# Kernel tuning notes

Measured on AMD Instinct MI355X. Metric: run time of the kernel, lower is better.

Reference implementation:

```python
import jax, jax.numpy as jnp
import numpy as np

C = 64
CQ = C // 4
G = 8  # group norm groups
EPS_GN = 1e-5
POS_COEF = 0.1


def setup_inputs() -> dict:
    key = jax.random.key(0)
    ks = jax.random.split(key, 12)
    B, N = 2, 4096
    return {
        "context_features": jax.random.normal(ks[0], (B, C, N), jnp.float32),
        "motion_features": jax.random.normal(ks[1], (B, C, N), jnp.float32),
        "xyz1": jax.random.uniform(ks[2], (B, N, 3), jnp.float32),
        # tied q/k conv weight (Conv1d k=1, no bias): (C//4, C)
        "Wqk": jax.random.normal(ks[3], (CQ, C), jnp.float32) * 0.1,
        # v_conv: Conv1d(C, C, 1) with bias
        "Wv": jax.random.normal(ks[4], (C, C), jnp.float32) * 0.1,
        "bv": jax.random.normal(ks[5], (C,), jnp.float32) * 0.1,
        # trans_conv: Conv1d(C, C, 1) with bias
        "Wt": jax.random.normal(ks[6], (C, C), jnp.float32) * 0.1,
        "bt": jax.random.normal(ks[7], (C,), jnp.float32) * 0.1,
        # GroupNorm(8, C) affine params
        "gn_w": jax.random.normal(ks[8], (C,), jnp.float32) * 0.1 + 1.0,
        "gn_b": jax.random.normal(ks[9], (C,), jnp.float32) * 0.1,
        # PReLU single slope, alpha_gma scalar (init 0 in torch; random here for testing)
        "prelu_a": jnp.float32(0.25) + jax.random.normal(ks[10], (), jnp.float32) * 0.01,
        "alpha": jax.random.normal(ks[11], (), jnp.float32) * 0.1,
    }


def _group_norm(x, w, b):
    # x: (B, C, N)
    B, Cc, N = x.shape
    xg = x.reshape(B, G, Cc // G, N)
    mu = xg.mean(axis=(2, 3), keepdims=True)
    var = xg.var(axis=(2, 3), keepdims=True)
    xn = ((xg - mu) * jax.lax.rsqrt(var + EPS_GN)).reshape(B, Cc, N)
    return xn * w[None, :, None] + b[None, :, None]


def reference(context_features, motion_features, xyz1, Wqk, Wv, bv, Wt, bt, gn_w, gn_b, prelu_a, alpha):
    # --- self attention (tied q/k) ---
    q = jnp.einsum("oc,bcn->bon", Wqk, context_features)  # (B, C/4, N)
    corr = jnp.einsum("bom,bon->bmn", q, q)               # (B, N, N)
    attn = jax.nn.softmax(corr, axis=-1)
    attn = attn / (1e-9 + attn.sum(axis=1, keepdims=True))

    # --- position mask via Gram-trick squared distances ---
    sq = jnp.sum(xyz1 * xyz1, axis=-1)                    # (B, N)
    d = sq[:, :, None] + sq[:, None, :] - 2.0 * jnp.einsum("bid,bjd->bij", xyz1, xyz1)
    d = jnp.maximum(d, 0.0)
    pos_am = d / (1e-9 + d.sum(axis=1, keepdims=True))
    mask = pos_am <= POS_COEF

    local = attn * mask
    local = jax.nn.softmax(local, axis=-1)
    local = local / (1e-9 + local.sum(axis=1, keepdims=True))
    attn = attn + local

    # --- GMA fusion ---
    xv = jnp.einsum("oc,bcn->bon", Wv, motion_features) + bv[None, :, None]
    gma = jnp.einsum("bcm,bmn->bcn", xv, attn)
    res = jnp.einsum("oc,bcn->bon", Wt, motion_features - gma) + bt[None, :, None]
    gr = _group_norm(res, gn_w, gn_b)
    gr = jnp.where(gr >= 0, gr, prelu_a * gr)  # PReLU
    return alpha * gr + motion_features
```

## Files before the change

### kernel.cpp

```cpp
#include <hip/hip_runtime.h>
#include <hip/hip_bf16.h>
#include <cstdio>

#define NB 2
#define NN 4096
#define NC 64
#define NQ 16
#define POS_COEF 0.1f

#define OFF_QT   0u
#define OFF_QK   131072u
#define OFF_XYZ4 262144u
#define OFF_XYZK 294912u
#define OFF_IRS1 327680u
#define OFF_IRS2 335872u
#define OFF_THR  344064u
#define OFF_ICS1 352256u
#define OFF_FLAG 360448u
#define OFF_XVB  360464u
#define OFF_SUMS 622608u
#define OFF_GN   622616u
#define OFF_CS2  622648u
#define OFF_GMA  630840u
#define OFF_G2   1155128u
#define WS_TOTAL 1679416u
#define ZERO_F   (WS_TOTAL - OFF_SUMS)
#define OFF_A0   1679424u
#define OFF_AE   18456640u
#define FULL_F   35233856u

using bf16x8 = __attribute__((ext_vector_type(8))) short;
using f32x4v = __attribute__((ext_vector_type(4))) float;

__device__ __forceinline__ float rcpf_(float x) { return __builtin_amdgcn_rcpf(x); }
__device__ __forceinline__ unsigned short f2bf(float x) {
  __hip_bfloat16 h = __float2bfloat16(x);
  return *(unsigned short*)&h;
}
__device__ __forceinline__ float bf2f(unsigned short u) {
  unsigned v = ((unsigned)u) << 16;
  return __builtin_bit_cast(float, v);
}

__device__ __forceinline__ float ldin(const void* p, size_t i, bool f32) {
  return f32 ? ((const float*)p)[i]
             : __bfloat162float(((const __hip_bfloat16*)p)[i]);
}

#define DOT16M(A0,A1,A2,A3,B0,B1,B2,B3) \
  fmaf((A0).x,(B0).x, fmaf((A0).y,(B0).y, fmaf((A0).z,(B0).z, fmaf((A0).w,(B0).w, \
  fmaf((A1).x,(B1).x, fmaf((A1).y,(B1).y, fmaf((A1).z,(B1).z, fmaf((A1).w,(B1).w, \
  fmaf((A2).x,(B2).x, fmaf((A2).y,(B2).y, fmaf((A2).z,(B2).z, fmaf((A2).w,(B2).w, \
  fmaf((A3).x,(B3).x, fmaf((A3).y,(B3).y, fmaf((A3).z,(B3).z, (A3).w*(B3).w)))))))))))))))

#define DOTC(M0,M1,M2,M3,C) \
  fmaf((M0).x,k0.C, fmaf((M0).y,k1.C, fmaf((M0).z,k2.C, fmaf((M0).w,k3.C, \
  fmaf((M1).x,k4.C, fmaf((M1).y,k5.C, fmaf((M1).z,k6.C, fmaf((M1).w,k7.C, \
  fmaf((M2).x,k8.C, fmaf((M2).y,k9.C, fmaf((M2).z,k10.C, fmaf((M2).w,k11.C, \
  fmaf((M3).x,k12.C, fmaf((M3).y,k13.C, fmaf((M3).z,k14.C, (M3).w*k15.C)))))))))))))))

#define LKPL(base, n0) \
  const float4 k0  = *(const float4*)((base) + 0*NN  + (n0)); \
  const float4 k1  = *(const float4*)((base) + 1*NN  + (n0)); \
  const float4 k2  = *(const float4*)((base) + 2*NN  + (n0)); \
  const float4 k3  = *(const float4*)((base) + 3*NN  + (n0)); \
  const float4 k4  = *(const float4*)((base) + 4*NN  + (n0)); \
  const float4 k5  = *(const float4*)((base) + 5*NN  + (n0)); \
  const float4 k6  = *(const float4*)((base) + 6*NN  + (n0)); \
  const float4 k7  = *(const float4*)((base) + 7*NN  + (n0)); \
  const float4 k8  = *(const float4*)((base) + 8*NN  + (n0)); \
  const float4 k9  = *(const float4*)((base) + 9*NN  + (n0)); \
  const float4 k10 = *(const float4*)((base) + 10*NN + (n0)); \
  const float4 k11 = *(const float4*)((base) + 11*NN + (n0)); \
  const float4 k12 = *(const float4*)((base) + 12*NN + (n0)); \
  const float4 k13 = *(const float4*)((base) + 13*NN + (n0)); \
  const float4 k14 = *(const float4*)((base) + 14*NN + (n0)); \
  const float4 k15 = *(const float4*)((base) + 15*NN + (n0));

#define WRED(s) { s += __shfl_xor(s, 32); s += __shfl_xor(s, 16); \
  s += __shfl_xor(s, 8); s += __shfl_xor(s, 4); s += __shfl_xor(s, 2); s += __shfl_xor(s, 1); }

#define LQROW(v, base) \
  const float4 v##0 = *(const float4*)((base)); \
  const float4 v##1 = *(const float4*)((base) + 4); \
  const float4 v##2 = *(const float4*)((base) + 8); \
  const float4 v##3 = *(const float4*)((base) + 12);

__global__ __launch_bounds__(256) void k0_detect(
    const unsigned short* __restrict__ ctx_u16, float* __restrict__ flag) {
  const int tid = threadIdx.x;
  int bad = 0;
  for (int i = tid; i < 8192; i += 256) {
    const unsigned short u = ctx_u16[i];
    const int e = (u >> 7) & 0xFF;
    if (e >= 134 || (e >= 1 && e <= 100)) bad++;
  }
  __shared__ int cnt;
  if (tid == 0) cnt = 0;
  __syncthreads();
  atomicAdd(&cnt, bad);
  __syncthreads();
  if (tid == 0) flag[0] = (cnt > 256) ? 1.0f : 0.0f;
}

__global__ __launch_bounds__(256) void k1_q_xyz(
    const void* __restrict__ ctx, const void* __restrict__ xyz,
    const void* __restrict__ wqk, const float* __restrict__ flag,
    float* __restrict__ qt, float* __restrict__ qk,
    float* __restrict__ xyz4, float* __restrict__ xyzk,
    float* __restrict__ sums) {
  const bool f32 = flag[0] > 0.5f;
  const int tid = threadIdx.x;
// ... 65 lines not shown
  float4 a1 = *(const float4*)(bvs + og * 16 + 4);
  float4 a2 = *(const float4*)(bvs + og * 16 + 8);
  float4 a3 = *(const float4*)(bvs + og * 16 + 12);
  const size_t mbase = (size_t)b * 64 * NN + n;
#pragma unroll 4
  for (int c = 0; c < 64; ++c) {
    float x = ldin(mot, mbase + (size_t)c * NN, f32);
    const float4 w0 = *(const float4*)(wvT + c * 64 + og * 16 + 0);
    const float4 w1 = *(const float4*)(wvT + c * 64 + og * 16 + 4);
    const float4 w2 = *(const float4*)(wvT + c * 64 + og * 16 + 8);
    const float4 w3 = *(const float4*)(wvT + c * 64 + og * 16 + 12);
    a0.x = fmaf(w0.x, x, a0.x); a0.y = fmaf(w0.y, x, a0.y); a0.z = fmaf(w0.z, x, a0.z); a0.w = fmaf(w0.w, x, a0.w);
    a1.x = fmaf(w1.x, x, a1.x); a1.y = fmaf(w1.y, x, a1.y); a1.z = fmaf(w1.z, x, a1.z); a1.w = fmaf(w1.w, x, a1.w);
    a2.x = fmaf(w2.x, x, a2.x); a2.y = fmaf(w2.y, x, a2.y); a2.z = fmaf(w2.z, x, a2.z); a2.w = fmaf(w2.w, x, a2.w);
    a3.x = fmaf(w3.x, x, a3.x); a3.y = fmaf(w3.y, x, a3.y); a3.z = fmaf(w3.z, x, a3.z); a3.w = fmaf(w3.w, x, a3.w);
  }
  unsigned short* xb = xvb + (size_t)b * 64 * NN + n;
  const int o0 = og * 16;
  xb[(size_t)(o0 + 0) * NN] = f2bf(a0.x);  xb[(size_t)(o0 + 1) * NN] = f2bf(a0.y);
  xb[(size_t)(o0 + 2) * NN] = f2bf(a0.z);  xb[(size_t)(o0 + 3) * NN] = f2bf(a0.w);
  xb[(size_t)(o0 + 4) * NN] = f2bf(a1.x);  xb[(size_t)(o0 + 5) * NN] = f2bf(a1.y);
  xb[(size_t)(o0 + 6) * NN] = f2bf(a1.z);  xb[(size_t)(o0 + 7) * NN] = f2bf(a1.w);
  xb[(size_t)(o0 + 8) * NN] = f2bf(a2.x);  xb[(size_t)(o0 + 9) * NN] = f2bf(a2.y);
  xb[(size_t)(o0 +10) * NN] = f2bf(a2.z);  xb[(size_t)(o0 +11) * NN] = f2bf(a2.w);
  xb[(size_t)(o0 +12) * NN] = f2bf(a3.x);  xb[(size_t)(o0 +13) * NN] = f2bf(a3.y);
  xb[(size_t)(o0 +14) * NN] = f2bf(a3.z);  xb[(size_t)(o0 +15) * NN] = f2bf(a3.w);
}

__global__ __launch_bounds__(256) void k2b_thr(
    const float* __restrict__ xyz4, const float* __restrict__ sums,
    float* __restrict__ thr) {
  const int idx = blockIdx.x * 256 + threadIdx.x;
  const int b = idx >> 12;
  const float4 pn = *(const float4*)(xyz4 + (size_t)idx * 4);
  const float Px = sums[b * 4 + 0], Py = sums[b * 4 + 1];
  const float Pz = sums[b * 4 + 2], S1 = sums[b * 4 + 3];
  float csd = fmaf((float)NN, pn.w, S1)
            - 2.f * (pn.x * Px + pn.y * Py + pn.z * Pz);
  thr[idx] = POS_COEF * (1e-9f + csd);
}


__global__ __launch_bounds__(256) void p1_rs1(
    const float* __restrict__ qt, const float* __restrict__ qk,
    float* __restrict__ irs1) {
  const int tid = threadIdx.x;
  const int b = blockIdx.x >> 8;
  const int m0 = (blockIdx.x & 255) << 4;
  const int w = tid >> 6, lane = tid & 63;
  const float* qb = qt + (size_t)b * NN * 16;
  const float* kb = qk + (size_t)b * 16 * NN;
  const int mA = m0 + w, mB = m0 + w + 4, mC = m0 + w + 8, mD = m0 + w + 12;
  LQROW(ma, qb + (size_t)mA * 16)
  LQROW(mb, qb + (size_t)mB * 16)
  LQROW(mc, qb + (size_t)mC * 16)
  LQROW(md, qb + (size_t)mD * 16)
  float sA = 0.f, sB = 0.f, sC = 0.f, sD = 0.f;
  for (int it = 0; it < 16; ++it) {
    const int n0 = (it << 8) + (lane << 2);
    LKPL(kb, n0)
    sA += __expf(fminf(DOTC(ma0,ma1,ma2,ma3,x), 80.f));
    sA += __expf(fminf(DOTC(ma0,ma1,ma2,ma3,y), 80.f));
    sA += __expf(fminf(DOTC(ma0,ma1,ma2,ma3,z), 80.f));
    sA += __expf(fminf(DOTC(ma0,ma1,ma2,ma3,w), 80.f));
    sB += __expf(fminf(DOTC(mb0,mb1,mb2,mb3,x), 80.f));
    sB += __expf(fminf(DOTC(mb0,mb1,mb2,mb3,y), 80.f));
    sB += __expf(fminf(DOTC(mb0,mb1,mb2,mb3,z), 80.f));
    sB += __expf(fminf(DOTC(mb0,mb1,mb2,mb3,w), 80.f));
    sC += __expf(fminf(DOTC(mc0,mc1,mc2,mc3,x), 80.f));
    sC += __expf(fminf(DOTC(mc0,mc1,mc2,mc3,y), 80.f));
    sC += __expf(fminf(DOTC(mc0,mc1,mc2,mc3,z), 80.f));
    sC += __expf(fminf(DOTC(mc0,mc1,mc2,mc3,w), 80.f));
    sD += __expf(fminf(DOTC(md0,md1,md2,md3,x), 80.f));
    sD += __expf(fminf(DOTC(md0,md1,md2,md3,y), 80.f));
    sD += __expf(fminf(DOTC(md0,md1,md2,md3,z), 80.f));
    sD += __expf(fminf(DOTC(md0,md1,md2,md3,w), 80.f));
  }
  WRED(sA) WRED(sB) WRED(sC) WRED(sD)
  if (lane == 0) {
    irs1[b * NN + mA] = rcpf_(sA);
    irs1[b * NN + mB] = rcpf_(sB);
    irs1[b * NN + mC] = rcpf_(sC);
    irs1[b * NN + mD] = rcpf_(sD);
  }
}

__global__ __launch_bounds__(256) void p3_rs2(
    const float* __restrict__ qt, const float* __restrict__ qk,
    const float* __restrict__ xyz4, const float* __restrict__ xyzk,
    const float* __restrict__ irs1, const float* __restrict__ ics1,
    const float* __restrict__ thr, float* __restrict__ irs2) {
  const int tid = threadIdx.x;
  const int b = blockIdx.x >> 8;
  const int m0 = (blockIdx.x & 255) << 4;
  const int w = tid >> 6, lane = tid & 63;
  const float* qb = qt + (size_t)b * NN * 16;
  const float* kb = qk + (size_t)b * 16 * NN;
  const float* xk = xyzk + (size_t)b * 4 * NN;
  const int mA = m0 + w, mB = m0 + w + 4, mC = m0 + w + 8, mD = m0 + w + 12;
  LQROW(ma, qb + (size_t)mA * 16)
  LQROW(mb, qb + (size_t)mB * 16)
  LQROW(mc, qb + (size_t)mC * 16)
  LQROW(md, qb + (size_t)mD * 16)
  const float4 pmA = *(const float4*)(xyz4 + ((size_t)b * NN + mA) * 4);
  const float4 pmB = *(const float4*)(xyz4 + ((size_t)b * NN + mB) * 4);
  const float4 pmC = *(const float4*)(xyz4 + ((size_t)b * NN + mC) * 4);
  const float4 pmD = *(const float4*)(xyz4 + ((size_t)b * NN + mD) * 4);
  const float rA = irs1[b * NN + mA];
  const float rB = irs1[b * NN + mB];
  const float rC = irs1[b * NN + mC];
  const float rD = irs1[b * NN + mD];
  float sA = 0.f, sB = 0.f, sC = 0.f, sD = 0.f;
#define P3C(S, M0,M1,M2,M3, PM, R, C) { \
    float corr_ = DOTC(M0,M1,M2,M3,C); \
    float a1v_ = __expf(fminf(corr_, 80.f)) * (R) * ic.C; \
    float dd_ = (PM).w + pw.C - 2.f * ((PM).x * px.C + (PM).y * py.C + (PM).z * pz.C); \
    dd_ = fmaxf(dd_, 0.f); \
    float l0_ = (dd_ <= th.C) ? a1v_ : 0.f; \
    S += __expf(l0_); }
  for (int it = 0; it < 16; ++it) {
    const int n0 = (it << 8) + (lane << 2);
    LKPL(kb, n0)
    const float4 px = *(const float4*)(xk + 0*NN + n0);
    const float4 py = *(const float4*)(xk + 1*NN + n0);
    const float4 pz = *(const float4*)(xk + 2*NN + n0);
    const float4 pw = *(const float4*)(xk + 3*NN + n0);
    const float4 ic = *(const float4*)(ics1 + b * NN + n0);
    const float4 th = *(const float4*)(thr + b * NN + n0);
    P3C(sA, ma0,ma1,ma2,ma3, pmA, rA, x)
    P3C(sA, ma0,ma1,ma2,ma3, pmA, rA, y)
    P3C(sA, ma0,ma1,ma2,ma3, pmA, rA, z)
    P3C(sA, ma0,ma1,ma2,ma3, pmA, rA, w)
    P3C(sB, mb0,mb1,mb2,mb3, pmB, rB, x)
    P3C(sB, mb0,mb1,mb2,mb3, pmB, rB, y)
    P3C(sB, mb0,mb1,mb2,mb3, pmB, rB, z)
    P3C(sB, mb0,mb1,mb2,mb3, pmB, rB, w)
    P3C(sC, mc0,mc1,mc2,mc3, pmC, rC, x)
    P3C(sC, mc0,mc1,mc2,mc3, pmC, rC, y)
    P3C(sC, mc0,mc1,mc2,mc3, pmC, rC, z)
    P3C(sC, mc0,mc1,mc2,mc3, pmC, rC, w)
    P3C(sD, md0,md1,md2,md3, pmD, rD, x)
    P3C(sD, md0,md1,md2,md3, pmD, rD, y)
    P3C(sD, md0,md1,md2,md3, pmD, rD, z)
    P3C(sD, md0,md1,md2,md3, pmD, rD, w)
  }
#undef P3C
  WRED(sA) WRED(sB) WRED(sC) WRED(sD)
  if (lane == 0) {
    irs2[b * NN + mA] = rcpf_(sA);
    irs2[b * NN + mB] = rcpf_(sB);
    irs2[b * NN + mC] = rcpf_(sC);
    irs2[b * NN + mD] = rcpf_(sD);
  }
}

__global__ __launch_bounds__(256) void k7_gma(
    const float* __restrict__ qt, const float* __restrict__ xyz4,
    const unsigned short* __restrict__ xvb,
    const float* __restrict__ irs1, const float* __restrict__ irs2,
    const float* __restrict__ ics1, const float* __restrict__ thr,
    float* __restrict__ g1, float* __restrict__ g2, float* __restrict__ cs2) {
  const int tid = threadIdx.x;
  const int bid = blockIdx.x;
  const int msl = bid & 7;
  const int nb = (bid >> 3) & 63;
  const int b = bid >> 9;
// ... 49 lines not shown
      COMPA(g * 4 + 3, u1.w, u2.w)
      *(ushort4*)(attns1 + ni * 72 + (aw << 4) + (g << 2)) = u1;
      *(ushort4*)(attns2 + ni * 72 + (aw << 4) + (g << 2)) = u2;
    }
    __syncthreads();
#pragma unroll
    for (int h = 0; h < 2; ++h) {
      const bf16x8 a1 = *(const bf16x8*)(attns1 + (nw + lr) * 72 + h * 32 + quad * 8);
      const bf16x8 a2 = *(const bf16x8*)(attns2 + (nw + lr) * 72 + h * 32 + quad * 8);
      const bf16x8 b0 = *(const bf16x8*)(xvs + (lr) * 72 + h * 32 + quad * 8);
      const bf16x8 b1 = *(const bf16x8*)(xvs + (16 + lr) * 72 + h * 32 + quad * 8);
      const bf16x8 b2 = *(const bf16x8*)(xvs + (32 + lr) * 72 + h * 32 + quad * 8);
      const bf16x8 b3 = *(const bf16x8*)(xvs + (48 + lr) * 72 + h * 32 + quad * 8);
      acc0 = __builtin_amdgcn_mfma_f32_16x16x32_bf16(a1, b0, acc0, 0, 0, 0);
      acc1 = __builtin_amdgcn_mfma_f32_16x16x32_bf16(a1, b1, acc1, 0, 0, 0);
      acc2 = __builtin_amdgcn_mfma_f32_16x16x32_bf16(a1, b2, acc2, 0, 0, 0);
      acc3 = __builtin_amdgcn_mfma_f32_16x16x32_bf16(a1, b3, acc3, 0, 0, 0);
      d0 = __builtin_amdgcn_mfma_f32_16x16x32_bf16(a2, b0, d0, 0, 0, 0);
      d1 = __builtin_amdgcn_mfma_f32_16x16x32_bf16(a2, b1, d1, 0, 0, 0);
      d2 = __builtin_amdgcn_mfma_f32_16x16x32_bf16(a2, b2, d2, 0, 0, 0);
      d3 = __builtin_amdgcn_mfma_f32_16x16x32_bf16(a2, b3, d3, 0, 0, 0);
    }
  }
#undef COMPA
  atomicAdd(&cs2[b * NN + na], csacc);
#define EPI(ACC, DST, CT) { \
    float* g_ = (DST) + ((size_t)b * NN + n0 + nw + (quad << 2)) * 64 + (CT) * 16 + lr; \
    atomicAdd(g_ + 0,   ACC[0]); \
    atomicAdd(g_ + 64,  ACC[1]); \
    atomicAdd(g_ + 128, ACC[2]); \
    atomicAdd(g_ + 192, ACC[3]); }
  EPI(acc0, g1, 0) EPI(acc1, g1, 1) EPI(acc2, g1, 2) EPI(acc3, g1, 3)
  EPI(d0, g2, 0) EPI(d1, g2, 1) EPI(d2, g2, 2) EPI(d3, g2, 3)
#undef EPI
}


__global__ __launch_bounds__(256) void p1w_rs1(
    const float* __restrict__ qt, const float* __restrict__ qk,
    float* __restrict__ irs1, unsigned short* __restrict__ a0g) {
  const int tid = threadIdx.x;
  const int b = blockIdx.x >> 8;
  const int m0 = (blockIdx.x & 255) << 4;
  const int w = tid >> 6, lane = tid & 63;
  const float* qb = qt + (size_t)b * NN * 16;
  const float* kb = qk + (size_t)b * 16 * NN;
  unsigned short* ab = a0g + (size_t)b * NN * NN;
  const int mA = m0 + w, mB = m0 + w + 4, mC = m0 + w + 8, mD = m0 + w + 12;
  LQROW(ma, qb + (size_t)mA * 16)
  LQROW(mb, qb + (size_t)mB * 16)
  LQROW(mc, qb + (size_t)mC * 16)
  LQROW(md, qb + (size_t)mD * 16)
  float sA = 0.f, sB = 0.f, sC = 0.f, sD = 0.f;
#define P1E(S, U, UC, M0,M1,M2,M3, C) { \
    float e_ = __expf(fminf(DOTC(M0,M1,M2,M3,C), 80.f)); \
    unsigned short us_ = f2bf(e_); U.UC = us_; S += bf2f(us_); }
  for (int it = 0; it < 16; ++it) {
    const int n0 = (it << 8) + (lane << 2);
    LKPL(kb, n0)
    ushort4 uA, uB, uC, uD;
    P1E(sA, uA, x, ma0,ma1,ma2,ma3, x) P1E(sA, uA, y, ma0,ma1,ma2,ma3, y)
    P1E(sA, uA, z, ma0,ma1,ma2,ma3, z) P1E(sA, uA, w, ma0,ma1,ma2,ma3, w)
    P1E(sB, uB, x, mb0,mb1,mb2,mb3, x) P1E(sB, uB, y, mb0,mb1,mb2,mb3, y)
    P1E(sB, uB, z, mb0,mb1,mb2,mb3, z) P1E(sB, uB, w, mb0,mb1,mb2,mb3, w)
    P1E(sC, uC, x, mc0,mc1,mc2,mc3, x) P1E(sC, uC, y, mc0,mc1,mc2,mc3, y)
    P1E(sC, uC, z, mc0,mc1,mc2,mc3, z) P1E(sC, uC, w, mc0,mc1,mc2,mc3, w)
    P1E(sD, uD, x, md0,md1,md2,md3, x) P1E(sD, uD, y, md0,md1,md2,md3, y)
    P1E(sD, uD, z, md0,md1,md2,md3, z) P1E(sD, uD, w, md0,md1,md2,md3, w)
    *(ushort4*)(ab + (size_t)mA * NN + n0) = uA;
    *(ushort4*)(ab + (size_t)mB * NN + n0) = uB;
    *(ushort4*)(ab + (size_t)mC * NN + n0) = uC;
    *(ushort4*)(ab + (size_t)mD * NN + n0) = uD;
  }
#undef P1E
  WRED(sA) WRED(sB) WRED(sC) WRED(sD)
  if (lane == 0) {
    irs1[b * NN + mA] = rcpf_(sA);
    irs1[b * NN + mB] = rcpf_(sB);
    irs1[b * NN + mC] = rcpf_(sC);
    irs1[b * NN + mD] = rcpf_(sD);
  }
}

__global__ __launch_bounds__(256) void p3w_rs2(
    const float* __restrict__ xyz4, const float* __restrict__ xyzk,
    const float* __restrict__ irs1, const float* __restrict__ ics1,
    const float* __restrict__ thr, float* __restrict__ irs2,
    const unsigned short* __restrict__ a0g, unsigned short* __restrict__ aeg) {
  const int tid = threadIdx.x;
  const int b = blockIdx.x >> 8;
  const int m0 = (blockIdx.x & 255) << 4;
  const int w = tid >> 6, lane = tid & 63;
  const float* xk = xyzk + (size_t)b * 4 * NN;
  const unsigned short* ab = a0g + (size_t)b * NN * NN;
  unsigned short* eb = aeg + (size_t)b * NN * NN;
  const int mA = m0 + w, mB = m0 + w + 4, mC = m0 + w + 8, mD = m0 + w + 12;
  const float4 pmA = *(const float4*)(xyz4 + ((size_t)b * NN + mA) * 4);
  const float4 pmB = *(const float4*)(xyz4 + ((size_t)b * NN + mB) * 4);
  const float4 pmC = *(const float4*)(xyz4 + ((size_t)b * NN + mC) * 4);
  const float4 pmD = *(const float4*)(xyz4 + ((size_t)b * NN + mD) * 4);
  const float rA = irs1[b * NN + mA];
  const float rB = irs1[b * NN + mB];
  const float rC = irs1[b * NN + mC];
  const float rD = irs1[b * NN + mD];
  float sA = 0.f, sB = 0.f, sC = 0.f, sD = 0.f;
#define P3W(S, RU, EU, UC, PM, R, C) { \
    float a1v_ = bf2f(RU.UC) * (R) * ic.C; \
    float dd_ = (PM).w + pw.C - 2.f * ((PM).x * px.C + (PM).y * py.C + (PM).z * pz.C); \
    dd_ = fmaxf(dd_, 0.f); \
    float l0_ = (dd_ <= th.C) ? a1v_ : 0.f; \
    unsigned short us_ = f2bf(__expf(l0_)); EU.UC = us_; S += bf2f(us_); }
  for (int it = 0; it < 16; ++it) {
    const int n0 = (it << 8) + (lane << 2);
    const float4 px = *(const float4*)(xk + 0*NN + n0);
    const float4 py = *(const float4*)(xk + 1*NN + n0);
    const float4 pz = *(const float4*)(xk + 2*NN + n0);
    const float4 pw = *(const float4*)(xk + 3*NN + n0);
    const float4 ic = *(const float4*)(ics1 + b * NN + n0);
    const float4 th = *(const float4*)(thr + b * NN + n0);
    const ushort4 rA4 = *(const ushort4*)(ab + (size_t)mA * NN + n0);
    const ushort4 rB4 = *(const ushort4*)(ab + (size_t)mB * NN + n0);
    const ushort4 rC4 = *(const ushort4*)(ab + (size_t)mC * NN + n0);
    const ushort4 rD4 = *(const ushort4*)(ab + (size_t)mD * NN + n0);
    ushort4 eA, eB, eC, eD;
    P3W(sA, rA4, eA, x, pmA, rA, x) P3W(sA, rA4, eA, y, pmA, rA, y)
    P3W(sA, rA4, eA, z, pmA, rA, z) P3W(sA, rA4, eA, w, pmA, rA, w)
    P3W(sB, rB4, eB, x, pmB, rB, x) P3W(sB, rB4, eB, y, pmB, rB, y)
    P3W(sB, rB4, eB, z, pmB, rB, z) P3W(sB, rB4, eB, w, pmB, rB, w)
    P3W(sC, rC4, eC, x, pmC, rC, x) P3W(sC, rC4, eC, y, pmC, rC, y)
    P3W(sC, rC4, eC, z, pmC, rC, z) P3W(sC, rC4, eC, w, pmC, rC, w)
    P3W(sD, rD4, eD, x, pmD, rD, x) P3W(sD, rD4, eD, y, pmD, rD, y)
    P3W(sD, rD4, eD, z, pmD, rD, z) P3W(sD, rD4, eD, w, pmD, rD, w)
    *(ushort4*)(eb + (size_t)mA * NN + n0) = eA;
    *(ushort4*)(eb + (size_t)mB * NN + n0) = eB;
    *(ushort4*)(eb + (size_t)mC * NN + n0) = eC;
    *(ushort4*)(eb + (size_t)mD * NN + n0) = eD;
  }
#undef P3W
  WRED(sA) WRED(sB) WRED(sC) WRED(sD)
  if (lane == 0) {
    irs2[b * NN + mA] = rcpf_(sA);
    irs2[b * NN + mB] = rcpf_(sB);
    irs2[b * NN + mC] = rcpf_(sC);
    irs2[b * NN + mD] = rcpf_(sD);
  }
}

__global__ __launch_bounds__(256) void k7f_gma(
    const unsigned short* __restrict__ a0g, const unsigned short* __restrict__ aeg,
    const unsigned short* __restrict__ xvb,
    const float* __restrict__ irs1, const float* __restrict__ irs2,
    const float* __restrict__ ics1,
    float* __restrict__ g1, float* __restrict__ g2, float* __restrict__ cs2) {
  const int tid = threadIdx.x;
  const int bid = blockIdx.x;
  const int msl = bid & 7;
  const int nb = (bid >> 3) & 63;
  const int b = bid >> 9;
  const int n0 = nb << 6;
  const int mstart = msl << 9;
  __shared__ __align__(16) unsigned short attns1[64 * 72];
  __shared__ __align__(16) unsigned short attns2[64 * 72];
  __shared__ __align__(16) unsigned short xvs[64 * 72];
  const unsigned short* ab = a0g + (size_t)b * NN * NN;
  const unsigned short* eb = aeg + (size_t)b * NN * NN;
  const int ni = tid & 63, aw = tid >> 6;
  const int na = n0 + ni;
  const float ics1n = ics1[b * NN + na];
  const int lane = tid & 63, wv = tid >> 6;
  const int lr = lane & 15, quad = lane >> 4;
  const int nw = wv << 4;
  f32x4v acc0 = {0,0,0,0}, acc1 = {0,0,0,0}, acc2 = {0,0,0,0}, acc3 = {0,0,0,0};
  f32x4v d0 = {0,0,0,0}, d1 = {0,0,0,0}, d2 = {0,0,0,0}, d3 = {0,0,0,0};
  float csacc = 0.f;
#define COMPF(MOFF, D1, D2) { \
    const int m_ = __builtin_amdgcn_readfirstlane(mw + (MOFF)); \
    float raw0_ = bf2f(ab[(size_t)m_ * NN + na]); \
    float rawe_ = bf2f(eb[(size_t)m_ * NN + na]); \
    float a1v_ = raw0_ * irs1[b * NN + m_] * ics1n; \
    float l2n_ = rawe_ * irs2[b * NN + m_]; \
    D1 = f2bf(a1v_); D2 = f2bf(l2n_); csacc += l2n_; }
  for (int mt = 0; mt < 8; ++mt) {
    const int m0 = mstart + (mt << 6);
    __syncthreads();
    {
      const int c = tid >> 2, part = tid & 3;
      const unsigned short* src = xvb + ((size_t)b * 64 + c) * NN + m0 + part * 16;
      unsigned short* dst = xvs + c * 72 + part * 16;
      *(uint4*)dst = *(const uint4*)src;
      *(uint4*)(dst + 8) = *(const uint4*)(src + 8);
    }
    const int mw = m0 + (aw << 4);
#pragma unroll
    for (int g = 0; g < 4; ++g) {
      ushort4 u1, u2;
      COMPF(g * 4 + 0, u1.x, u2.x)
      COMPF(g * 4 + 1, u1.y, u2.y)
      COMPF(g * 4 + 2, u1.z, u2.z)
      COMPF(g * 4 + 3, u1.w, u2.w)
      *(ushort4*)(attns1 + ni * 72 + (aw << 4) + (g << 2)) = u1;
      *(ushort4*)(attns2 + ni * 72 + (aw << 4) + (g << 2)) = u2;
    }
    __syncthreads();
#pragma unroll
    for (int h = 0; h < 2; ++h) {
      const bf16x8 a1 = *(const bf16x8*)(attns1 + (nw + lr) * 72 + h * 32 + quad * 8);
      const bf16x8 a2 = *(const bf16x8*)(attns2 + (nw + lr) * 72 + h * 32 + quad * 8);
      const bf16x8 b0 = *(const bf16x8*)(xvs + (lr) * 72 + h * 32 + quad * 8);
      const bf16x8 b1 = *(const bf16x8*)(xvs + (16 + lr) * 72 + h * 32 + quad * 8);
      const bf16x8 b2 = *(const bf16x8*)(xvs + (32 + lr) * 72 + h * 32 + quad * 8);
      const bf16x8 b3 = *(const bf16x8*)(xvs + (48 + lr) * 72 + h * 32 + quad * 8);
      acc0 = __builtin_amdgcn_mfma_f32_16x16x32_bf16(a1, b0, acc0, 0, 0, 0);
      acc1 = __builtin_amdgcn_mfma_f32_16x16x32_bf16(a1, b1, acc1, 0, 0, 0);
      acc2 = __builtin_amdgcn_mfma_f32_16x16x32_bf16(a1, b2, acc2, 0, 0, 0);
      acc3 = __builtin_amdgcn_mfma_f32_16x16x32_bf16(a1, b3, acc3, 0, 0, 0);
      d0 = __builtin_amdgcn_mfma_f32_16x16x32_bf16(a2, b0, d0, 0, 0, 0);
      d1 = __builtin_amdgcn_mfma_f32_16x16x32_bf16(a2, b1, d1, 0, 0, 0);
      d2 = __builtin_amdgcn_mfma_f32_16x16x32_bf16(a2, b2, d2, 0, 0, 0);
      d3 = __builtin_amdgcn_mfma_f32_16x16x32_bf16(a2, b3, d3, 0, 0, 0);
    }
  }
#undef COMPF
  atomicAdd(&cs2[b * NN + na], csacc);
#define EPI(ACC, DST, CT) { \
    float* g_ = (DST) + ((size_t)b * NN + n0 + nw + (quad << 2)) * 64 + (CT) * 16 + lr; \
    atomicAdd(g_ + 0,   ACC[0]); \
    atomicAdd(g_ + 64,  ACC[1]); \
    atomicAdd(g_ + 128, ACC[2]); \
    atomicAdd(g_ + 192, ACC[3]); }
  EPI(acc0, g1, 0) EPI(acc1, g1, 1) EPI(acc2, g1, 2) EPI(acc3, g1, 3)
  EPI(d0, g2, 0) EPI(d1, g2, 1) EPI(d2, g2, 2) EPI(d3, g2, 3)
#undef EPI
}


__global__ __launch_bounds__(256) void p2_cs1(
    const float* __restrict__ qt, const float* __restrict__ qk,
    const float* __restrict__ irs1, float* __restrict__ ics1) {
  const int tid = threadIdx.x;
  const int b = blockIdx.x >> 8;
  const int n0t = (blockIdx.x & 255) << 4;
  const int w = tid >> 6, lane = tid & 63;
  const float* qb = qt + (size_t)b * NN * 16;
  const float* kb = qk + (size_t)b * 16 * NN;
  const int nA = n0t + w, nB = n0t + w + 4, nC = n0t + w + 8, nD = n0t + w + 12;
  LQROW(na, qb + (size_t)nA * 16)
  LQROW(nb, qb + (size_t)nB * 16)
  LQROW(nc, qb + (size_t)nC * 16)
  LQROW(nd, qb + (size_t)nD * 16)
  float sA = 0.f, sB = 0.f, sC = 0.f, sD = 0.f;
  for (int it = 0; it < 16; ++it) {
    const int m0 = (it << 8) + (lane << 2);
    LKPL(kb, m0)
    const float4 r1 = *(const float4*)(irs1 + b * NN + m0);
    sA = fmaf(__expf(fminf(DOTC(na0,na1,na2,na3,x), 80.f)), r1.x, sA);
    sA = fmaf(__expf(fminf(DOTC(na0,na1,na2,na3,y), 80.f)), r1.y, sA);
    sA = fmaf(__expf(fminf(DOTC(na0,na1,na2,na3,z), 80.f)), r1.z, sA);
    sA = fmaf(__expf(fminf(DOTC(na0,na1,na2,na3,w), 80.f)), r1.w, sA);
    sB = fmaf(__expf(fminf(DOTC(nb0,nb1,nb2,nb3,x), 80.f)), r1.x, sB);
    sB = fmaf(__expf(fminf(DOTC(nb0,nb1,nb2,nb3,y), 80.f)), r1.y, sB);
    sB = fmaf(__expf(fminf(DOTC(nb0,nb1,nb2,nb3,z), 80.f)), r1.z, sB);
    sB = fmaf(__expf(fminf(DOTC(nb0,nb1,nb2,nb3,w), 80.f)), r1.w, sB);
    sC = fmaf(__expf(fminf(DOTC(nc0,nc1,nc2,nc3,x), 80.f)), r1.x, sC);
    sC = fmaf(__expf(fminf(DOTC(nc0,nc1,nc2,nc3,y), 80.f)), r1.y, sC);
    sC = fmaf(__expf(fminf(DOTC(nc0,nc1,nc2,nc3,z), 80.f)), r1.z, sC);
    sC = fmaf(__expf(fminf(DOTC(nc0,nc1,nc2,nc3,w), 80.f)), r1.w, sC);
    sD = fmaf(__expf(fminf(DOTC(nd0,nd1,nd2,nd3,x), 80.f)), r1.x, sD);
    sD = fmaf(__expf(fminf(DOTC(nd0,nd1,nd2,nd3,y), 80.f)), r1.y, sD);
    sD = fmaf(__expf(fminf(DOTC(nd0,nd1,nd2,nd3,z), 80.f)), r1.z, sD);
    sD = fmaf(__expf(fminf(DOTC(nd0,nd1,nd2,nd3,w), 80.f)), r1.w, sD);
  }
  WRED(sA) WRED(sB) WRED(sC) WRED(sD)
  if (lane == 0) {
    ics1[b * NN + nA] = rcpf_(1e-9f + sA);
    ics1[b * NN + nB] = rcpf_(1e-9f + sB);
    ics1[b * NN + nC] = rcpf_(1e-9f + sC);
    ics1[b * NN + nD] = rcpf_(1e-9f + sD);
  }
}

__global__ __launch_bounds__(256) void k8_res(
    const void* __restrict__ mot, const void* __restrict__ wt,
    const void* __restrict__ bt, const float* __restrict__ flag,
    float* __restrict__ g1_res, const float* __restrict__ g2,
    const float* __restrict__ cs2, float* __restrict__ gn) {
  const bool f32 = flag[0] > 0.5f;
  const int tid = threadIdx.x;
  const int bid = blockIdx.x;
  const int b = bid >> 9;
  const int n0 = (bid & 511) << 3;
  __shared__ float wtT[64 * 65];
  __shared__ float bts[64];
  __shared__ float md[8 * 64];
  __shared__ float gs[8], gss[8];
  for (int i = tid; i < 4096; i += 256) {
    int o = i & 63, c = i >> 6;
    wtT[c * 65 + o] = ldin(wt, o * 64 + c, f32);
  }
  if (tid < 64) bts[tid] = ldin(bt, tid, f32);
  if (tid < 8) { gs[tid] = 0.f; gss[tid] = 0.f; }
#pragma unroll
  for (int r = 0; r < 2; ++r) {
    const int idx = tid * 2 + r;
    const int c = idx & 63, nl = idx >> 6;
    const size_t gi = ((size_t)b * NN + n0 + nl) * 64 + c;
    const float ics2n = rcpf_(1e-9f + cs2[b * NN + n0 + nl]);
    float gmav = fmaf(g2[gi], ics2n, g1_res[gi]);
    md[nl * 64 + c] = ldin(mot, ((size_t)b * 64 + c) * NN + n0 + nl, f32) - gmav;
  }
  __syncthreads();
  const int o = tid & 63, ng = tid >> 6;
  const int nl0 = ng * 2, nl1 = ng * 2 + 1;
  float a0 = bts[o], a1 = bts[o];
#pragma unroll 8
  for (int c = 0; c < 64; ++c) {
    float w = wtT[c * 65 + o];
    a0 = fmaf(w, md[nl0 * 64 + c], a0);
    a1 = fmaf(w, md[nl1 * 64 + c], a1);
  }
  g1_res[((size_t)b * NN + n0 + nl0) * 64 + o] = a0;
  g1_res[((size_t)b * NN + n0 + nl1) * 64 + o] = a1;
  atomicAdd(&gs[o >> 3], a0 + a1);
  atomicAdd(&gss[o >> 3], a0 * a0 + a1 * a1);
  __syncthreads();
  if (tid < 8) atomicAdd(&gn[b * 8 + tid], gs[tid]);
  else if (tid < 16) atomicAdd(&gn[16 + b * 8 + (tid - 8)], gss[tid - 8]);
}

__global__ __launch_bounds__(256) void k9_out(
    const float* __restrict__ res, const float* __restrict__ gn,
    const void* __restrict__ mot,
    const void* __restrict__ gnw, const void* __restrict__ gnb,
    const void* __restrict__ pa, const void* __restrict__ al,
    const float* __restrict__ flag, void* __restrict__ out) {
  const bool f32 = flag[0] > 0.5f;
  const int idx = blockIdx.x * 256 + threadIdx.x;
  const int n = idx & 4095;
  const int c = (idx >> 12) & 63;
  const int b = idx >> 18;
  const int g = c >> 3;
  const float inv_cnt = 1.f / 32768.f;
  float mean = gn[b * 8 + g] * inv_cnt;
  float var = gn[16 + b * 8 + g] * inv_cnt - mean * mean;
  var = fmaxf(var, 0.f);
  float rstd = rsqrtf(var + 1e-5f);
  float r = res[((size_t)b * NN + n) * 64 + c];
  float y = (r - mean) * rstd * ldin(gnw, c, f32) + ldin(gnb, c, f32);
  float slope = ldin(pa, 0, f32);
  y = (y >= 0.f) ? y : slope * y;
  float o = ldin(al, 0, f32) * y + ldin(mot, idx, f32);
  if (f32) ((float*)out)[idx] = o;
  else     ((__hip_bfloat16*)out)[idx] = __float2bfloat16(o);
}

extern "C" void kernel_launch(void* const* d_in, const int* in_sizes, int n_in,
                              void* d_out, int out_size, void* d_ws, size_t ws_size,
                              hipStream_t stream) {
  const void* ctx = d_in[0];
  const void* mot = d_in[1];
  const void* xyz = d_in[2];
  const void* wqk = d_in[3];
  const void* wv  = d_in[4];
  const void* bv  = d_in[5];
  const void* wt  = d_in[6];
  const void* bt  = d_in[7];
  const void* gnw = d_in[8];
  const void* gnb = d_in[9];
  const void* pa  = d_in[10];
  const void* al  = d_in[11];
  float* ws = (float*)d_ws;
  const bool big = ws_size >= (size_t)FULL_F * sizeof(float);

  if (ws_size < (size_t)WS_TOTAL * sizeof(float))
    fprintf(stderr, "[gma3d] WARNING ws_size=%zu < needed %zu\n",
            ws_size, (size_t)WS_TOTAL * sizeof(float));

  hipMemsetAsync(ws + OFF_SUMS, 0, (size_t)ZERO_F * sizeof(float), stream);

  k0_detect<<<1, 256, 0, stream>>>((const unsigned short*)ctx, ws + OFF_FLAG);
  k1_q_xyz<<<32, 256, 0, stream>>>(ctx, xyz, wqk, ws + OFF_FLAG,
                                   ws + OFF_QT, ws + OFF_QK,
                                   ws + OFF_XYZ4, ws + OFF_XYZK, ws + OFF_SUMS);
  k2_xv<<<128, 256, 0, stream>>>(mot, wv, bv, ws + OFF_FLAG,
                                 (unsigned short*)(ws + OFF_XVB));
  k2b_thr<<<32, 256, 0, stream>>>(ws + OFF_XYZ4, ws + OFF_SUMS, ws + OFF_THR);

  if (big) {
    unsigned short* a0 = (unsigned short*)(ws + OFF_A0);
    unsigned short* ae = (unsigned short*)(ws + OFF_AE);
    p1w_rs1<<<512, 256, 0, stream>>>(ws + OFF_QT, ws + OFF_QK, ws + OFF_IRS1, a0);
    p2_cs1<<<512, 256, 0, stream>>>(ws + OFF_QT, ws + OFF_QK, ws + OFF_IRS1, ws + OFF_ICS1);
    p3w_rs2<<<512, 256, 0, stream>>>(ws + OFF_XYZ4, ws + OFF_XYZK,
                                     ws + OFF_IRS1, ws + OFF_ICS1, ws + OFF_THR,
                                     ws + OFF_IRS2, a0, ae);
    k7f_gma<<<1024, 256, 0, stream>>>(a0, ae,
                                      (const unsigned short*)(ws + OFF_XVB),
                                      ws + OFF_IRS1, ws + OFF_IRS2, ws + OFF_ICS1,
                                      ws + OFF_GMA, ws + OFF_G2, ws + OFF_CS2);
  } else {
    p1_rs1<<<512, 256, 0, stream>>>(ws + OFF_QT, ws + OFF_QK, ws + OFF_IRS1);
    p2_cs1<<<512, 256, 0, stream>>>(ws + OFF_QT, ws + OFF_QK, ws + OFF_IRS1, ws + OFF_ICS1);
    p3_rs2<<<512, 256, 0, stream>>>(ws + OFF_QT, ws + OFF_QK,
                                    ws + OFF_XYZ4, ws + OFF_XYZK,
                                    ws + OFF_IRS1, ws + OFF_ICS1, ws + OFF_THR,
                                    ws + OFF_IRS2);
    k7_gma<<<1024, 256, 0, stream>>>(ws + OFF_QT, ws + OFF_XYZ4,
                                     (const unsigned short*)(ws + OFF_XVB),
                                     ws + OFF_IRS1, ws + OFF_IRS2,
                                     ws + OFF_ICS1, ws + OFF_THR,
                                     ws + OFF_GMA, ws + OFF_G2, ws + OFF_CS2);
  }

  k8_res<<<1024, 256, 0, stream>>>(mot, wt, bt, ws + OFF_FLAG,
                                   ws + OFF_GMA, ws + OFF_G2, ws + OFF_CS2, ws + OFF_GN);
  k9_out<<<2048, 256, 0, stream>>>(ws + OFF_GMA, ws + OFF_GN, mot, gnw, gnb, pa, al,
                                   ws + OFF_FLAG, d_out);
}
```

Measured before the change: 330.1 us.

## Drop second stored attention matrix and compute column sums from stored bf16 matrix

The path with a large workspace no longer writes and reads a second N×N bf16 matrix of local-softmax exponentials. k7h now recomputes the position mask and exp from xyz and the threshold. Column sums of the normalized attention are now built by a streaming pass over the stored bf16 matrix with atomic adds, instead of recomputing the QK dot products and exponentials. This trades N² memory traffic for extra exp and distance arithmetic in the GMA kernel, and the column sums now come from bf16-rounded values.

```diff
diff --git a/kernel.cpp b/kernel.cpp
--- a/kernel.cpp
+++ b/kernel.cpp
@@ -21,13 +21,13 @@
 #define OFF_SUMS 622608u
 #define OFF_GN   622616u
 #define OFF_CS2  622648u
-#define OFF_GMA  630840u
-#define OFF_G2   1155128u
-#define WS_TOTAL 1679416u
+#define OFF_CS1G 630840u
+#define OFF_GMA  639032u
+#define OFF_G2   1163320u
+#define WS_TOTAL 1687608u
 #define ZERO_F   (WS_TOTAL - OFF_SUMS)
-#define OFF_A0   1679424u
-#define OFF_AE   18456640u
-#define FULL_F   35233856u
+#define OFF_A0   1687616u
+#define FULL_F   18464832u
 
 using bf16x8 = __attribute__((ext_vector_type(8))) short;
 using f32x4v = __attribute__((ext_vector_type(4))) float;
@@ -259,6 +259,51 @@
     irs1[b * NN + mB] = rcpf_(sB);
     irs1[b * NN + mC] = rcpf_(sC);
     irs1[b * NN + mD] = rcpf_(sD);
+  }
+}
+
+__global__ __launch_bounds__(256) void p2_cs1(
+    const float* __restrict__ qt, const float* __restrict__ qk,
+    const float* __restrict__ irs1, float* __restrict__ ics1) {
+  const int tid = threadIdx.x;
+  const int b = blockIdx.x >> 8;
+  const int n0t = (blockIdx.x & 255) << 4;
+  const int w = tid >> 6, lane = tid & 63;
+  const float* qb = qt + (size_t)b * NN * 16;
+  const float* kb = qk + (size_t)b * 16 * NN;
+  const int nA = n0t + w, nB = n0t + w + 4, nC = n0t + w + 8, nD = n0t + w + 12;
+  LQROW(na, qb + (size_t)nA * 16)
+  LQROW(nb, qb + (size_t)nB * 16)
+  LQROW(nc, qb + (size_t)nC * 16)
+  LQROW(nd, qb + (size_t)nD * 16)
+  float sA = 0.f, sB = 0.f, sC = 0.f, sD = 0.f;
+  for (int it = 0; it < 16; ++it) {
+    const int m0 = (it << 8) + (lane << 2);
+    LKPL(kb, m0)
+    const float4 r1 = *(const float4*)(irs1 + b * NN + m0);
+    sA = fmaf(__expf(fminf(DOTC(na0,na1,na2,na3,x), 80.f)), r1.x, sA);
+    sA = fmaf(__expf(fminf(DOTC(na0,na1,na2,na3,y), 80.f)), r1.y, sA);
+    sA = fmaf(__expf(fminf(DOTC(na0,na1,na2,na3,z), 80.f)), r1.z, sA);
+    sA = fmaf(__expf(fminf(DOTC(na0,na1,na2,na3,w), 80.f)), r1.w, sA);
+    sB = fmaf(__expf(fminf(DOTC(nb0,nb1,nb2,nb3,x), 80.f)), r1.x, sB);
+    sB = fmaf(__expf(fminf(DOTC(nb0,nb1,nb2,nb3,y), 80.f)), r1.y, sB);
+    sB = fmaf(__expf(fminf(DOTC(nb0,nb1,nb2,nb3,z), 80.f)), r1.z, sB);
+    sB = fmaf(__expf(fminf(DOTC(nb0,nb1,nb2,nb3,w), 80.f)), r1.w, sB);
+    sC = fmaf(__expf(fminf(DOTC(nc0,nc1,nc2,nc3,x), 80.f)), r1.x, sC);
+    sC = fmaf(__expf(fminf(DOTC(nc0,nc1,nc2,nc3,y), 80.f)), r1.y, sC);
+    sC = fmaf(__expf(fminf(DOTC(nc0,nc1,nc2,nc3,z), 80.f)), r1.z, sC);
+    sC = fmaf(__expf(fminf(DOTC(nc0,nc1,nc2,nc3,w), 80.f)), r1.w, sC);
+    sD = fmaf(__expf(fminf(DOTC(nd0,nd1,nd2,nd3,x), 80.f)), r1.x, sD);
+    sD = fmaf(__expf(fminf(DOTC(nd0,nd1,nd2,nd3,y), 80.f)), r1.y, sD);
+    sD = fmaf(__expf(fminf(DOTC(nd0,nd1,nd2,nd3,z), 80.f)), r1.z, sD);
+    sD = fmaf(__expf(fminf(DOTC(nd0,nd1,nd2,nd3,w), 80.f)), r1.w, sD);
+  }
+  WRED(sA) WRED(sB) WRED(sC) WRED(sD)
+  if (lane == 0) {
+    ics1[b * NN + nA] = rcpf_(1e-9f + sA);
+    ics1[b * NN + nB] = rcpf_(1e-9f + sB);
+    ics1[b * NN + nC] = rcpf_(1e-9f + sC);
+    ics1[b * NN + nD] = rcpf_(1e-9f + sD);
   }
 }
 
@@ -474,18 +519,41 @@
   }
 }
 
-__global__ __launch_bounds__(256) void p3w_rs2(
+__global__ __launch_bounds__(256) void p2s_cs1(
+    const unsigned short* __restrict__ a0g, const float* __restrict__ irs1,
+    float* __restrict__ cs1g) {
+  const int bid = blockIdx.x;
+  const int ms = bid & 7;
+  const int ng = (bid >> 3) & 15;
+  const int b = bid >> 7;
+  const int n = (ng << 8) + threadIdx.x;
+  const unsigned short* ab = a0g + (size_t)b * NN * NN + n;
+  const float* r1 = irs1 + b * NN;
+  float acc = 0.f;
+  const int m0 = ms << 9;
+#pragma unroll 8
+  for (int m = m0; m < m0 + 512; ++m)
+    acc = fmaf(bf2f(ab[(size_t)m * NN]), r1[m], acc);
+  atomicAdd(&cs1g[b * NN + n], acc);
+}
+
+__global__ __launch_bounds__(256) void k2c_ics1(
+    const float* __restrict__ cs1g, float* __restrict__ ics1) {
+  const int idx = blockIdx.x * 256 + threadIdx.x;
+  ics1[idx] = rcpf_(1e-9f + cs1g[idx]);
+}
+
+__global__ __launch_bounds__(256) void p3v_rs2(
     const float* __restrict__ xyz4, const float* __restrict__ xyzk,
     const float* __restrict__ irs1, const float* __restrict__ ics1,
     const float* __restrict__ thr, float* __restrict__ irs2,
-    const unsigned short* __restrict__ a0g, unsigned short* __restrict__ aeg) {
+    const unsigned short* __restrict__ a0g) {
   const int tid = threadIdx.x;
   const int b = blockIdx.x >> 8;
   const int m0 = (blockIdx.x & 255) << 4;
   const int w = tid >> 6, lane = tid & 63;
   const float* xk = xyzk + (size_t)b * 4 * NN;
   const unsigned short* ab = a0g + (size_t)b * NN * NN;
-  unsigned short* eb = aeg + (size_t)b * NN * NN;
   const int mA = m0 + w, mB = m0 + w + 4, mC = m0 + w + 8, mD = m0 + w + 12;
   const float4 pmA = *(const float4*)(xyz4 + ((size_t)b * NN + mA) * 4);
   const float4 pmB = *(const float4*)(xyz4 + ((size_t)b * NN + mB) * 4);
@@ -496,12 +564,12 @@
   const float rC = irs1[b * NN + mC];
   const float rD = irs1[b * NN + mD];
   float sA = 0.f, sB = 0.f, sC = 0.f, sD = 0.f;
-#define P3W(S, RU, EU, UC, PM, R, C) { \
+#define P3V(S, RU, UC, PM, R, C) { \
     float a1v_ = bf2f(RU.UC) * (R) * ic.C; \
     float dd_ = (PM).w + pw.C - 2.f * ((PM).x * px.C + (PM).y * py.C + (PM).z * pz.C); \
     dd_ = fmaxf(dd_, 0.f); \
     float l0_ = (dd_ <= th.C) ? a1v_ : 0.f; \
-    unsigned short us_ = f2bf(__expf(l0_)); EU.UC = us_; S += bf2f(us_); }
+    S += __expf(l0_); }
   for (int it = 0; it < 16; ++it) {
     const int n0 = (it << 8) + (lane << 2);
     const float4 px = *(const float4*)(xk + 0*NN + n0);
@@ -514,21 +582,16 @@
     const ushort4 rB4 = *(const ushort4*)(ab + (size_t)mB * NN + n0);
     const ushort4 rC4 = *(const ushort4*)(ab + (size_t)mC * NN + n0);
     const ushort4 rD4 = *(const ushort4*)(ab + (size_t)mD * NN + n0);
-    ushort4 eA, eB, eC, eD;
-    P3W(sA, rA4, eA, x, pmA, rA, x) P3W(sA, rA4, eA, y, pmA, rA, y)
-    P3W(sA, rA4, eA, z, pmA, rA, z) P3W(sA, rA4, eA, w, pmA, rA, w)
-    P3W(sB, rB4, eB, x, pmB, rB, x) P3W(sB, rB4, eB, y, pmB, rB, y)
-    P3W(sB, rB4, eB, z, pmB, rB, z) P3W(sB, rB4, eB, w, pmB, rB, w)
-    P3W(sC, rC4, eC, x, pmC, rC, x) P3W(sC, rC4, eC, y, pmC, rC, y)
-    P3W(sC, rC4, eC, z, pmC, rC, z) P3W(sC, rC4, eC, w, pmC, rC, w)
-    P3W(sD, rD4, eD, x, pmD, rD, x) P3W(sD, rD4, eD, y, pmD, rD, y)
-    P3W(sD, rD4, eD, z, pmD, rD, z) P3W(sD, rD4, eD, w, pmD, rD, w)
-    *(ushort4*)(eb + (size_t)mA * NN + n0) = eA;
-    *(ushort4*)(eb + (size_t)mB * NN + n0) = eB;
-    *(ushort4*)(eb + (size_t)mC * NN + n0) = eC;
-    *(ushort4*)(eb + (size_t)mD * NN + n0) = eD;
-  }
-#undef P3W
+    P3V(sA, rA4, x, pmA, rA, x) P3V(sA, rA4, y, pmA, rA, y)
+    P3V(sA, rA4, z, pmA, rA, z) P3V(sA, rA4, w, pmA, rA, w)
+    P3V(sB, rB4, x, pmB, rB, x) P3V(sB, rB4, y, pmB, rB, y)
+    P3V(sB, rB4, z, pmB, rB, z) P3V(sB, rB4, w, pmB, rB, w)
+    P3V(sC, rC4, x, pmC, rC, x) P3V(sC, rC4, y, pmC, rC, y)
+    P3V(sC, rC4, z, pmC, rC, z) P3V(sC, rC4, w, pmC, rC, w)
+    P3V(sD, rD4, x, pmD, rD, x) P3V(sD, rD4, y, pmD, rD, y)
+    P3V(sD, rD4, z, pmD, rD, z) P3V(sD, rD4, w, pmD, rD, w)
+  }
+#undef P3V
   WRED(sA) WRED(sB) WRED(sC) WRED(sD)
   if (lane == 0) {
     irs2[b * NN + mA] = rcpf_(sA);
@@ -538,11 +601,11 @@
   }
 }
 
-__global__ __launch_bounds__(256) void k7f_gma(
-    const unsigned short* __restrict__ a0g, const unsigned short* __restrict__ aeg,
+__global__ __launch_bounds__(256) void k7h_gma(
+    const unsigned short* __restrict__ a0g, const float* __restrict__ xyz4,
     const unsigned short* __restrict__ xvb,
     const float* __restrict__ irs1, const float* __restrict__ irs2,
-    const float* __restrict__ ics1,
+    const float* __restrict__ ics1, const float* __restrict__ thr,
     float* __restrict__ g1, float* __restrict__ g2, float* __restrict__ cs2) {
   const int tid = threadIdx.x;
   const int bid = blockIdx.x;
@@ -555,22 +618,27 @@
   __shared__ __align__(16) unsigned short attns2[64 * 72];
   __shared__ __align__(16) unsigned short xvs[64 * 72];
   const unsigned short* ab = a0g + (size_t)b * NN * NN;
-  const unsigned short* eb = aeg + (size_t)b * NN * NN;
+  const float* pb = xyz4 + (size_t)b * NN * 4;
   const int ni = tid & 63, aw = tid >> 6;
   const int na = n0 + ni;
+  const float4 pn = *(const float4*)(pb + (size_t)na * 4);
   const float ics1n = ics1[b * NN + na];
+  const float thr_n = thr[b * NN + na];
   const int lane = tid & 63, wv = tid >> 6;
   const int lr = lane & 15, quad = lane >> 4;
   const int nw = wv << 4;
   f32x4v acc0 = {0,0,0,0}, acc1 = {0,0,0,0}, acc2 = {0,0,0,0}, acc3 = {0,0,0,0};
   f32x4v d0 = {0,0,0,0}, d1 = {0,0,0,0}, d2 = {0,0,0,0}, d3 = {0,0,0,0};
   float csacc = 0.f;
-#define COMPF(MOFF, D1, D2) { \
+#define COMPH(MOFF, D1, D2) { \
     const int m_ = __builtin_amdgcn_readfirstlane(mw + (MOFF)); \
-    float raw0_ = bf2f(ab[(size_t)m_ * NN + na]); \
-    float rawe_ = bf2f(eb[(size_t)m_ * NN + na]); \
-    float a1v_ = raw0_ * irs1[b * NN + m_] * ics1n; \
-    float l2n_ = rawe_ * irs2[b * NN + m_]; \
+    float raw_ = bf2f(ab[(size_t)m_ * NN + na]); \
+    const float4 pm_ = *(const float4*)(pb + (size_t)m_ * 4); \
+    float a1v_ = raw_ * irs1[b * NN + m_] * ics1n; \
+    float dd_ = pm_.w + pn.w - 2.f * (pm_.x * pn.x + pm_.y * pn.y + pm_.z * pn.z); \
+    dd_ = fmaxf(dd_, 0.f); \
+    float l0_ = (dd_ <= thr_n) ? a1v_ : 0.f; \
+    float l2n_ = __expf(l0_) * irs2[b * NN + m_]; \
     D1 = f2bf(a1v_); D2 = f2bf(l2n_); csacc += l2n_; }
   for (int mt = 0; mt < 8; ++mt) {
     const int m0 = mstart + (mt << 6);
@@ -586,10 +654,10 @@
 #pragma unroll
     for (int g = 0; g < 4; ++g) {
       ushort4 u1, u2;
-      COMPF(g * 4 + 0, u1.x, u2.x)
-      COMPF(g * 4 + 1, u1.y, u2.y)
-      COMPF(g * 4 + 2, u1.z, u2.z)
-      COMPF(g * 4 + 3, u1.w, u2.w)
+      COMPH(g * 4 + 0, u1.x, u2.x)
+      COMPH(g * 4 + 1, u1.y, u2.y)
+      COMPH(g * 4 + 2, u1.z, u2.z)
+      COMPH(g * 4 + 3, u1.w, u2.w)
       *(ushort4*)(attns1 + ni * 72 + (aw << 4) + (g << 2)) = u1;
       *(ushort4*)(attns2 + ni * 72 + (aw << 4) + (g << 2)) = u2;
     }
@@ -612,7 +680,7 @@
       d3 = __builtin_amdgcn_mfma_f32_16x16x32_bf16(a2, b3, d3, 0, 0, 0);
     }
   }
-#undef COMPF
+#undef COMPH
   atomicAdd(&cs2[b * NN + na], csacc);
 #define EPI(ACC, DST, CT) { \
     float* g_ = (DST) + ((size_t)b * NN + n0 + nw + (quad << 2)) * 64 + (CT) * 16 + lr; \
@@ -625,51 +693,6 @@
 #undef EPI
 }
 
-
-__global__ __launch_bounds__(256) void p2_cs1(
-    const float* __restrict__ qt, const float* __restrict__ qk,
-    const float* __restrict__ irs1, float* __restrict__ ics1) {
-  const int tid = threadIdx.x;
-  const int b = blockIdx.x >> 8;
-  const int n0t = (blockIdx.x & 255) << 4;
-  const int w = tid >> 6, lane = tid & 63;
-  const float* qb = qt + (size_t)b * NN * 16;
-  const float* kb = qk + (size_t)b * 16 * NN;
-  const int nA = n0t + w, nB = n0t + w + 4, nC = n0t + w + 8, nD = n0t + w + 12;
-  LQROW(na, qb + (size_t)nA * 16)
-  LQROW(nb, qb + (size_t)nB * 16)
-  LQROW(nc, qb + (size_t)nC * 16)
-  LQROW(nd, qb + (size_t)nD * 16)
-  float sA = 0.f, sB = 0.f, sC = 0.f, sD = 0.f;
-  for (int it = 0; it < 16; ++it) {
-    const int m0 = (it << 8) + (lane << 2);
-    LKPL(kb, m0)
-    const float4 r1 = *(const float4*)(irs1 + b * NN + m0);
-    sA = fmaf(__expf(fminf(DOTC(na0,na1,na2,na3,x), 80.f)), r1.x, sA);
-    sA = fmaf(__expf(fminf(DOTC(na0,na1,na2,na3,y), 80.f)), r1.y, sA);
-    sA = fmaf(__expf(fminf(DOTC(na0,na1,na2,na3,z), 80.f)), r1.z, sA);
-    sA = fmaf(__expf(fminf(DOTC(na0,na1,na2,na3,w), 80.f)), r1.w, sA);
-    sB = fmaf(__expf(fminf(DOTC(nb0,nb1,nb2,nb3,x), 80.f)), r1.x, sB);
-    sB = fmaf(__expf(fminf(DOTC(nb0,nb1,nb2,nb3,y), 80.f)), r1.y, sB);
-    sB = fmaf(__expf(fminf(DOTC(nb0,nb1,nb2,nb3,z), 80.f)), r1.z, sB);
-    sB = fmaf(__expf(fminf(DOTC(nb0,nb1,nb2,nb3,w), 80.f)), r1.w, sB);
-    sC = fmaf(__expf(fminf(DOTC(nc0,nc1,nc2,nc3,x), 80.f)), r1.x, sC);
-    sC = fmaf(__expf(fminf(DOTC(nc0,nc1,nc2,nc3,y), 80.f)), r1.y, sC);
-    sC = fmaf(__expf(fminf(DOTC(nc0,nc1,nc2,nc3,z), 80.f)), r1.z, sC);
-    sC = fmaf(__expf(fminf(DOTC(nc0,nc1,nc2,nc3,w), 80.f)), r1.w, sC);
-    sD = fmaf(__expf(fminf(DOTC(nd0,nd1,nd2,nd3,x), 80.f)), r1.x, sD);
-    sD = fmaf(__expf(fminf(DOTC(nd0,nd1,nd2,nd3,y), 80.f)), r1.y, sD);
-    sD = fmaf(__expf(fminf(DOTC(nd0,nd1,nd2,nd3,z), 80.f)), r1.z, sD);
-    sD = fmaf(__expf(fminf(DOTC(nd0,nd1,nd2,nd3,w), 80.f)), r1.w, sD);
-  }
-  WRED(sA) WRED(sB) WRED(sC) WRED(sD)
-  if (lane == 0) {
-    ics1[b * NN + nA] = rcpf_(1e-9f + sA);
-    ics1[b * NN + nB] = rcpf_(1e-9f + sB);
-    ics1[b * NN + nC] = rcpf_(1e-9f + sC);
-    ics1[b * NN + nD] = rcpf_(1e-9f + sD);
-  }
-}
 
 __global__ __launch_bounds__(256) void k8_res(
     const void* __restrict__ mot, const void* __restrict__ wt,
@@ -779,15 +802,16 @@
 
   if (big) {
     unsigned short* a0 = (unsigned short*)(ws + OFF_A0);
-    unsigned short* ae = (unsigned short*)(ws + OFF_AE);
     p1w_rs1<<<512, 256, 0, stream>>>(ws + OFF_QT, ws + OFF_QK, ws + OFF_IRS1, a0);
-    p2_cs1<<<512, 256, 0, stream>>>(ws + OFF_QT, ws + OFF_QK, ws + OFF_IRS1, ws + OFF_ICS1);
-    p3w_rs2<<<512, 256, 0, stream>>>(ws + OFF_XYZ4, ws + OFF_XYZK,
+    p2s_cs1<<<256, 256, 0, stream>>>(a0, ws + OFF_IRS1, ws + OFF_CS1G);
+    k2c_ics1<<<32, 256, 0, stream>>>(ws + OFF_CS1G, ws + OFF_ICS1);
+    p3v_rs2<<<512, 256, 0, stream>>>(ws + OFF_XYZ4, ws + OFF_XYZK,
                                      ws + OFF_IRS1, ws + OFF_ICS1, ws + OFF_THR,
-                                     ws + OFF_IRS2, a0, ae);
-    k7f_gma<<<1024, 256, 0, stream>>>(a0, ae,
+                                     ws + OFF_IRS2, a0);
+    k7h_gma<<<1024, 256, 0, stream>>>(a0, ws + OFF_XYZ4,
                                       (const unsigned short*)(ws + OFF_XVB),
-                                      ws + OFF_IRS1, ws + OFF_IRS2, ws + OFF_ICS1,
+                                      ws + OFF_IRS1, ws + OFF_IRS2,
+                                      ws + OFF_ICS1, ws + OFF_THR,
                                       ws + OFF_GMA, ws + OFF_G2, ws + OFF_CS2);
   } else {
     p1_rs1<<<512, 256, 0, stream>>>(ws + OFF_QT, ws + OFF_QK, ws + OFF_IRS1);
```

Result: no change. 330.3 us (+0.1%).
